# Kernel tuning notes

Hardware: AMD Instinct MI355X
Metric: run time of the kernel (lower is better)

## Reference

```python
import jax, jax.numpy as jnp
import numpy as np

K = 20  # neighbors, per get_u_xt default


def setup_inputs() -> dict:
    key = jax.random.key(0)
    ks = jax.random.split(key, 6)
    B, N, D, H = 2048, 100000, 64, 256
    return {
        "t": jax.random.uniform(ks[0], (1,), dtype=jnp.float32),
        "z": jax.random.normal(ks[1], (B, D + 2), dtype=jnp.float32),
        "data": jax.random.normal(ks[2], (N, D), dtype=jnp.float32),
        "velocity": jax.random.normal(ks[3], (N, D), dtype=jnp.float32),
        "W1": jax.random.normal(ks[4], (D + 1, H), dtype=jnp.float32) * 0.05,
        "b1": jnp.zeros((H,), dtype=jnp.float32),
        "W2": jax.random.normal(ks[5], (H, D), dtype=jnp.float32) * 0.05,
        "b2": jnp.zeros((D,), dtype=jnp.float32),
    }


def _get_u_xt(xt, x, v, k=K):
    # Euclidean cdist via ||a||^2 + ||b||^2 - 2 a.b  -> [B, N]
    sq = (jnp.sum(xt * xt, axis=1)[:, None]
          + jnp.sum(x * x, axis=1)[None, :]
          - 2.0 * (xt @ x.T))
    dists = jnp.sqrt(jnp.maximum(sq, 1e-30))
    neg_d, knn_idx = jax.lax.top_k(-dists, k)  # k smallest distances
    knn_dists = -neg_d                          # ascending order, [B, k]
    h = jnp.maximum(knn_dists[:, -1:], 1e-12)   # bandwidth = k-th NN dist
    w = jnp.exp(-knn_dists ** 2 / (2.0 * h ** 2))
    w = w / (jnp.sum(w, axis=1, keepdims=True) + 1e-12)
    v_knn = v[knn_idx]                          # gather [B, k, D]
    return jnp.einsum('bk,bkd->bd', w, v_knn)


def reference(t, z, data, velocity, W1, b1, W2, b2):
    x = z[:, :-2]                               # [B, D]
    B = x.shape[0]
    inp = jnp.concatenate([x, jnp.broadcast_to(t, (B,))[:, None]], axis=1)
    x_dot = jax.nn.relu(inp @ W1 + b1) @ W2 + b2  # MLP model(...) -> [B, D]
    u_t = _get_u_xt(x, data, velocity)
    eps = 1e-8  # torch F.cosine_similarity eps
    nu = jnp.maximum(jnp.linalg.norm(u_t, axis=1), eps)
    nx = jnp.maximum(jnp.linalg.norm(x_dot, axis=1), eps)
    cos_sim = 1.0 - jnp.sum(u_t * x_dot, axis=1) / (nu * nx)
    L2_squared = jnp.sum((u_t - x_dot) ** 2, axis=1)
    return jnp.concatenate([x_dot, cos_sim[:, None], L2_squared[:, None]], axis=1)
```

## Files before the change

kernel.cpp:

```cpp
#include <hip/hip_runtime.h>
#include <math.h>

#define B      2048
#define N      100000
#define NPAD2  100352
#define JGRP2  98
#define JT4    16
#define DD     64
#define HH     256
#define KK     20
#define SAMPLE 8192
#define CAP    1024
#define SSEL   512
#define SLACK  1.5f
#define LCAP   16

#define INF_F (__builtin_inff())

typedef __bf16 bf16x8 __attribute__((ext_vector_type(8)));
typedef __bf16 bf16x4 __attribute__((ext_vector_type(4)));
typedef float  floatx4 __attribute__((ext_vector_type(4)));
union U16 { uint4 u; bf16x8 v; };

__device__ __forceinline__ float wsum64(float v) {
    #pragma unroll
    for (int o = 32; o > 0; o >>= 1) v += __shfl_xor(v, o, 64);
    return v;
}
__device__ __forceinline__ int wsum64i(int v) {
    #pragma unroll
    for (int o = 32; o > 0; o >>= 1) v += __shfl_xor(v, o, 64);
    return v;
}

#define NB_DATA 6272
#define NB_PREP 512
#define NB_MLP  256
__global__ __launch_bounds__(256) void setup_all(const float* __restrict__ z,
                                                 const float* __restrict__ tp,
                                                 const float* __restrict__ data,
                                                 const float* __restrict__ W1,
                                                 const float* __restrict__ b1,
                                                 const float* __restrict__ W2,
                                                 const float* __restrict__ b2,
                                                 float* __restrict__ xs,
                                                 float* __restrict__ xnorm,
                                                 __bf16* __restrict__ xs_h,
                                                 int* __restrict__ cnt,
                                                 float* __restrict__ dnorm,
                                                 float* __restrict__ dnh,
                                                 __bf16* __restrict__ d_hi,
                                                 float* __restrict__ xdot) {
    int bx = blockIdx.x, tid = threadIdx.x;
    if (bx < NB_DATA) {
        int gt = bx * 256 + tid;
        int j = gt >> 4, l = gt & 15;
        float4 v = make_float4(0.f, 0.f, 0.f, 0.f);
        if (j < N)
            v = reinterpret_cast<const float4*>(data + (size_t)j * 64)[l];
        bf16x4 o;
        o.x = (__bf16)v.x; o.y = (__bf16)v.y; o.z = (__bf16)v.z; o.w = (__bf16)v.w;
        *reinterpret_cast<bf16x4*>(d_hi + (size_t)j * 64 + l * 4) = o;
        float s = v.x * v.x + v.y * v.y + v.z * v.z + v.w * v.w;
        #pragma unroll
        for (int o2 = 1; o2 < 16; o2 <<= 1) s += __shfl_xor(s, o2, 64);
        if (l == 0) {
            dnorm[j] = (j < N) ? s : INF_F;
            dnh[j]   = (j < N) ? 0.5f * s : INF_F;
        }
    } else if (bx < NB_DATA + NB_PREP) {
        int row = (bx - NB_DATA) * 4 + (tid >> 6);
        int d = tid & 63;
        float v = z[row * 66 + d];
        xs[row * 64 + d] = v;
        xs_h[row * 64 + d] = (__bf16)v;
        float s = wsum64(v * v);
        if (d == 0) xnorm[row] = s;
        if (d == 1) cnt[row] = 0;
    } else {
        __shared__ float sin_[8][65];
        __shared__ float shid[8][HH];
        int row0 = (bx - NB_DATA - NB_PREP) * 8;
        float tval = tp[0];
        for (int idx = tid; idx < 8 * 64; idx += 256) {
            int r = idx >> 6, d = idx & 63;
            sin_[r][d] = z[(row0 + r) * 66 + d];
        }
        if (tid < 8) sin_[tid][64] = tval;
        __syncthreads();
        int h = tid;
        float acc[8];
        #pragma unroll
        for (int r = 0; r < 8; ++r) acc[r] = b1[h];
        for (int i = 0; i < 65; ++i) {
            float wv = W1[i * HH + h];
            #pragma unroll
            for (int r = 0; r < 8; ++r) acc[r] = fmaf(sin_[r][i], wv, acc[r]);
        }
        #pragma unroll
        for (int r = 0; r < 8; ++r) shid[r][h] = fmaxf(acc[r], 0.f);
        __syncthreads();
        int d = tid & 63, rb = tid >> 6;
        for (int rr = rb; rr < 8; rr += 4) {
            float a = b2[d];
            #pragma unroll 8
            for (int hh2 = 0; hh2 < HH; ++hh2)
                a = fmaf(shid[rr][hh2], W2[hh2 * 64 + d], a);
            xdot[(size_t)(row0 + rr) * 64 + d] = a;
        }
    }
}

__global__ __launch_bounds__(256) void sample_gemm(const __bf16* __restrict__ xs_h,
                                                   const __bf16* __restrict__ d_hi,
                                                   const float* __restrict__ xnorm,
                                                   const float* __restrict__ dnorm,
                                                   unsigned short* __restrict__ samp16) {
    int tid = threadIdx.x;
    int m0 = blockIdx.x * 128;
    int jbase = blockIdx.y * 128;
    int wv = tid >> 6, wm = wv & 1, wn = wv >> 1;
    int lane = tid & 63, l16 = lane & 15, quad = lane >> 4;

    bf16x8 af[2][4], bfr[2][4];
    #pragma unroll
    for (int s = 0; s < 2; ++s)
        #pragma unroll
        for (int mt = 0; mt < 4; ++mt) {
            int row = m0 + wm * 64 + mt * 16 + l16;
            U16 u; u.u = reinterpret_cast<const uint4*>(xs_h + (size_t)row * 64)[s * 4 + quad];
            af[s][mt] = u.v;
        }
    #pragma unroll
    for (int s = 0; s < 2; ++s)
        #pragma unroll
        for (int nt = 0; nt < 4; ++nt) {
            int jr = jbase + wn * 64 + nt * 16 + l16;
            U16 u; u.u = reinterpret_cast<const uint4*>(d_hi + (size_t)jr * 64)[s * 4 + quad];
            bfr[s][nt] = u.v;
        }
    float dn[4], sxn[4][4];
    #pragma unroll
    for (int nt = 0; nt < 4; ++nt)
        dn[nt] = dnorm[jbase + wn * 64 + nt * 16 + l16];
    #pragma unroll
    for (int mt = 0; mt < 4; ++mt)
        #pragma unroll
        for (int rg = 0; rg < 4; ++rg)
            sxn[mt][rg] = xnorm[m0 + wm * 64 + mt * 16 + quad * 4 + rg];

    floatx4 acc[4][4];
    #pragma unroll
    for (int mt = 0; mt < 4; ++mt)
        #pragma unroll
        for (int nt = 0; nt < 4; ++nt)
            acc[mt][nt] = (floatx4){0.f, 0.f, 0.f, 0.f};
    #pragma unroll
    for (int s = 0; s < 2; ++s)
        #pragma unroll
        for (int mt = 0; mt < 4; ++mt)
            #pragma unroll
            for (int nt = 0; nt < 4; ++nt)
                acc[mt][nt] = __builtin_amdgcn_mfma_f32_16x16x32_bf16(
                    af[s][mt], bfr[s][nt], acc[mt][nt], 0, 0, 0);

    #pragma unroll
    for (int mt = 0; mt < 4; ++mt)
        #pragma unroll
        for (int nt = 0; nt < 4; ++nt) {
            floatx4 a4 = acc[mt][nt];
            int j = jbase + wn * 64 + nt * 16 + l16;
            #pragma unroll
            for (int rg = 0; rg < 4; ++rg) {
                int row = m0 + wm * 64 + mt * 16 + quad * 4 + rg;
                float sq = fmaf(a4[rg], -2.f, dn[nt]) + sxn[mt][rg];
                samp16[(size_t)row * SAMPLE + j] =
                    (unsigned short)(__float_as_uint(fmaxf(sq, 0.f)) >> 16);
            }
        }
}

__global__ __launch_bounds__(256) void thr_select(const unsigned short* __restrict__ samp16,
                                                  float* __restrict__ thr) {
    int wv = threadIdx.x >> 6, lane = threadIdx.x & 63;
    int row = blockIdx.x * 4 + wv;
    const unsigned* sp = reinterpret_cast<const unsigned*>(samp16 + (size_t)row * SAMPLE);
    unsigned w[64];
    #pragma unroll
    for (int i = 0; i < 64; ++i) w[i] = sp[lane + i * 64];
    unsigned res = 0;
    for (int b = 15; b >= 0; --b) {
        unsigned cand = res | (1u << b);
        int c = 0;
        #pragma unroll
        for (int i = 0; i < 64; ++i) {
            c += ((w[i] & 0xFFFFu) < cand);
            c += ((w[i] >> 16) < cand);
        }
        c = wsum64i(c);
        if (c <= KK - 1) res = cand;
    }
    if (lane == 0) thr[row] = __uint_as_float((res + 1u) << 16);
}

__global__ __launch_bounds__(256, 3) void gemm_filter(const __bf16* __restrict__ xs_h,
                                                      const __bf16* __restrict__ d_hi,
                                                      const float* __restrict__ xnorm,
                                                      const float* __restrict__ dnh,
                                                      const float* __restrict__ thr,
                                                      int* __restrict__ cnt,
                                                      float* __restrict__ bufd,
                                                      int* __restrict__ bufi) {
    __shared__ float sts[128];
    __shared__ int   lcnt[128];
    __shared__ float lbd[128][LCAP + 1];
    __shared__ int   lbj[128][LCAP + 1];
    int tid = threadIdx.x;
    int m0 = blockIdx.x * 128;
    int jstart = blockIdx.y * (JT4 * 64);
    int wv = tid >> 6, wm = wv & 1, wn = wv >> 1;
    int lane = tid & 63, l16 = lane & 15, quad = lane >> 4;

    if (tid < 128) {
        sts[tid] = thr[m0 + tid] + 2.0f * SLACK;
        lcnt[tid] = 0;
    }
    bf16x8 af[2][4];
    #pragma unroll
    for (int s = 0; s < 2; ++s)
        #pragma unroll
        for (int mt = 0; mt < 4; ++mt) {
            int row = m0 + wm * 64 + mt * 16 + l16;
            U16 u; u.u = reinterpret_cast<const uint4*>(xs_h + (size_t)row * 64)[s * 4 + quad];
            af[s][mt] = u.v;
        }
    float scv[4][4];
    #pragma unroll
    for (int mt = 0; mt < 4; ++mt)
        #pragma unroll
        for (int rg = 0; rg < 4; ++rg) {
            int mg = m0 + wm * 64 + mt * 16 + quad * 4 + rg;
            scv[mt][rg] = 0.5f * (thr[mg] + 2.0f * SLACK - xnorm[mg]);
        }
    __syncthreads();

    uint4 bb[2][4];
    float dh[2][2];
    {
        #pragma unroll
        for (int s = 0; s < 2; ++s)
            #pragma unroll
            for (int nt = 0; nt < 2; ++nt) {
                int jr = jstart + wn * 32 + nt * 16 + l16;
                bb[0][s * 2 + nt] = reinterpret_cast<const uint4*>(d_hi + (size_t)jr * 64)[s * 4 + quad];
            }
        #pragma unroll
        for (int nt = 0; nt < 2; ++nt)
            dh[0][nt] = dnh[jstart + wn * 32 + nt * 16 + l16];
    }

    #pragma unroll 2
    for (int t = 0; t < JT4; ++t) {
        int cur = t & 1, nxt = cur ^ 1;
        if (t + 1 < JT4) {
            int jb = jstart + (t + 1) * 64;
            #pragma unroll
            for (int s = 0; s < 2; ++s)
                #pragma unroll
                for (int nt = 0; nt < 2; ++nt) {
                    int jr = jb + wn * 32 + nt * 16 + l16;
                    bb[nxt][s * 2 + nt] = reinterpret_cast<const uint4*>(d_hi + (size_t)jr * 64)[s * 4 + quad];
                }
            #pragma unroll
            for (int nt = 0; nt < 2; ++nt)
                dh[nxt][nt] = dnh[jb + wn * 32 + nt * 16 + l16];
        }

        floatx4 acc[4][2];
        #pragma unroll
        for (int mt = 0; mt < 4; ++mt) {
            floatx4 cv = (floatx4){scv[mt][0], scv[mt][1], scv[mt][2], scv[mt][3]};
            acc[mt][0] = cv;
            acc[mt][1] = cv;
        }
        #pragma unroll
        for (int s = 0; s < 2; ++s) {
            U16 u0, u1;
            u0.u = bb[cur][s * 2 + 0];
            u1.u = bb[cur][s * 2 + 1];
            #pragma unroll
            for (int mt = 0; mt < 4; ++mt) {
                acc[mt][0] = __builtin_amdgcn_mfma_f32_16x16x32_bf16(af[s][mt], u0.v, acc[mt][0], 0, 0, 0);
                acc[mt][1] = __builtin_amdgcn_mfma_f32_16x16x32_bf16(af[s][mt], u1.v, acc[mt][1], 0, 0, 0);
            }
        }

        int jb = jstart + t * 64;
        #pragma unroll
        for (int nt = 0; nt < 2; ++nt) {
            int j = jb + wn * 32 + nt * 16 + l16;
            float dd = dh[cur][nt];
            #pragma unroll
            for (int mt = 0; mt < 4; ++mt) {
                floatx4 a4 = acc[mt][nt];
                bool p0 = a4[0] >= dd, p1 = a4[1] >= dd;
                bool p2 = a4[2] >= dd, p3 = a4[3] >= dd;
                if (p0 | p1 | p2 | p3) {
                    #pragma unroll
                    for (int rg = 0; rg < 4; ++rg) {
                        bool pp = (rg == 0) ? p0 : (rg == 1) ? p1 : (rg == 2) ? p2 : p3;
                        if (pp) {
                            int mloc = wm * 64 + mt * 16 + quad * 4 + rg;
                            float delta = 2.0f * (dd - a4[rg]);
                            int pos = atomicAdd(&lcnt[mloc], 1);
                            if (pos < LCAP) {
                                lbd[mloc][pos] = delta;
                                lbj[mloc][pos] = j;
                            } else {
                                int row = m0 + mloc;
                                int gp = atomicAdd(&cnt[row], 1);
                                if (gp < CAP) {
                                    bufd[(size_t)row * CAP + gp] = sts[mloc] + delta;
                                    bufi[(size_t)row * CAP + gp] = j;
                                }
                            }
                        }
                    }
                }
            }
        }
    }
    __syncthreads();
    if (tid < 128) {
        int c = lcnt[tid];
        if (c > LCAP) c = LCAP;
        if (c > 0) {
            int row = m0 + tid;
            float ts = sts[tid];
            int base = atomicAdd(&cnt[row], c);
            for (int i = 0; i < c; ++i) {
                int gp = base + i;
                if (gp < CAP) {
                    bufd[(size_t)row * CAP + gp] = ts + lbd[tid][i];
                    bufi[(size_t)row * CAP + gp] = lbj[tid][i];
                }
            }
        }
    }
}

__global__ __launch_bounds__(64) void select_finish(const float* __restrict__ bufd,
                                                    const int* __restrict__ bufi,
                                                    const int* __restrict__ cnt,
                                                    const float* __restrict__ xs,
                                                    const float* __restrict__ xnorm,
                                                    const float* __restrict__ dnorm,
                                                    const float* __restrict__ data,
                                                    const float* __restrict__ xdot,
                                                    const float* __restrict__ vel,
                                                    float* __restrict__ out) {
    __shared__ float sd[CAP];
    __shared__ int   si[CAP];
    __shared__ float sx[64];
    __shared__ float se[SSEL];
    __shared__ int   sj[SSEL];
    __shared__ int   scnt;
    __shared__ float seld[KK];
    __shared__ int   seli[KK];
    __shared__ float selw[KK];
    int row = blockIdx.x, lane = threadIdx.x;
    int n = cnt[row];
    if (n > CAP) n = CAP;
    for (int i = lane; i < n; i += 64) {
        sd[i] = bufd[(size_t)row * CAP + i];
        si[i] = bufi[(size_t)row * CAP + i];
    }
    sx[lane] = xs[row * 64 + lane];
    if (lane == 0) scnt = 0;
    __syncthreads();

    unsigned res = 0;
    for (int b = 30; b >= 0; --b) {
        unsigned cand = res | (1u << b);
        int c = 0;
        for (int i = lane; i < n; i += 64)
            c += (__float_as_uint(fmaxf(sd[i], 0.f)) < cand);
        c = wsum64i(c);
        if (c <= KK - 1) res = cand;
    }
    float T = __uint_as_float(res);

    for (int i = lane; i < n; i += 64) {
        if (sd[i] <= T + 2.0f * SLACK) {
            int q = atomicAdd(&scnt, 1);
            if (q < SSEL) sj[q] = si[i];
        }
    }
    __syncthreads();
    int m = scnt < SSEL ? scnt : SSEL;
    for (int c = lane; c < m; c += 64) {
        int j = sj[c];
        const float4* dp = reinterpret_cast<const float4*>(data + (size_t)j * 64);
        float dot = 0.f;
        #pragma unroll
        for (int kb = 0; kb < 16; ++kb) {
            float4 q = dp[kb];
            dot = fmaf(sx[kb * 4 + 0], q.x, dot);
            dot = fmaf(sx[kb * 4 + 1], q.y, dot);
            dot = fmaf(sx[kb * 4 + 2], q.z, dot);
            dot = fmaf(sx[kb * 4 + 3], q.w, dot);
        }
        se[c] = xnorm[row] + dnorm[j] - 2.0f * dot;
    }
    __syncthreads();
    for (int k = 0; k < KK; ++k) {
        float v = INF_F; int id = 0x7fffffff; int p = -1;
        for (int i = lane; i < m; i += 64) {
            float x = se[i]; int xi = sj[i];
            if (x < v || (x == v && xi < id)) { v = x; id = xi; p = i; }
        }
        #pragma unroll
        for (int o = 32; o > 0; o >>= 1) {
            float ov = __shfl_xor(v, o, 64);
            int oid = __shfl_xor(id, o, 64);
            int op  = __shfl_xor(p, o, 64);
            if (ov < v || (ov == v && oid < id)) { v = ov; id = oid; p = op; }
        }
        if (lane == 0) {
            seld[k] = v; seli[k] = id;
            if (p >= 0) se[p] = INF_F;
        }
        __syncthreads();
    }
    float d20 = sqrtf(fmaxf(seld[KK - 1], 1e-30f));
    float h = fmaxf(d20, 1e-12f);
    float wk = 0.f;
    if (lane < KK) {
        float dd = sqrtf(fmaxf(seld[lane], 1e-30f));
        wk = expf(-(dd * dd) / (2.f * h * h));
    }
    float tot = wsum64(wk) + 1e-12f;
    if (lane < KK) selw[lane] = wk / tot;
    __syncthreads();
    float u = 0.f;
    #pragma unroll
    for (int k = 0; k < KK; ++k)
        u = fmaf(selw[k], vel[(size_t)seli[k] * 64 + lane], u);
    float xd = xdot[(size_t)row * 64 + lane];
    float du  = wsum64(u * xd);
    float nu2 = wsum64(u * u);
    float nx2 = wsum64(xd * xd);
    float l2  = wsum64((u - xd) * (u - xd));
    float nu = fmaxf(sqrtf(nu2), 1e-8f);
    float nx = fmaxf(sqrtf(nx2), 1e-8f);
    out[(size_t)row * 66 + lane] = xd;
    if (lane == 0) {
        out[(size_t)row * 66 + 64] = 1.f - du / (nu * nx);
        out[(size_t)row * 66 + 65] = l2;
    }
}

extern "C" void kernel_launch(void* const* d_in, const int* in_sizes, int n_in,
                              void* d_out, int out_size, void* d_ws, size_t ws_size,
                              hipStream_t stream) {
    const float* t_   = (const float*)d_in[0];
    const float* z    = (const float*)d_in[1];
    const float* data = (const float*)d_in[2];
    const float* vel  = (const float*)d_in[3];
    const float* W1   = (const float*)d_in[4];
    const float* b1   = (const float*)d_in[5];
    const float* W2   = (const float*)d_in[6];
    const float* b2   = (const float*)d_in[7];
    float* out = (float*)d_out;

    float*  xs    = (float*)d_ws;
    float*  xnorm = xs + 131072;
    float*  thr   = xnorm + 2048;
    int*    cnt   = (int*)(thr + 2048);
    float*  xdot  = (float*)(cnt + 2048);
    float*  dnorm = xdot + 131072;
    float*  dnh   = dnorm + NPAD2;
    __bf16* xs_h  = (__bf16*)(dnh + NPAD2);
    __bf16* d_hi  = xs_h + 131072;
    unsigned short* samp16 = (unsigned short*)(d_hi + (size_t)NPAD2 * 64);
    float*  bufd  = (float*)samp16;
    int*    bufi  = (int*)(bufd + (size_t)B * CAP);

    setup_all<<<NB_DATA + NB_PREP + NB_MLP, 256, 0, stream>>>(
        z, t_, data, W1, b1, W2, b2, xs, xnorm, xs_h, cnt, dnorm, dnh, d_hi, xdot);
    sample_gemm<<<dim3(B / 128, SAMPLE / 128), 256, 0, stream>>>(xs_h, d_hi, xnorm, dnorm, samp16);
    thr_select<<<B / 4, 256, 0, stream>>>(samp16, thr);
    gemm_filter<<<dim3(B / 128, JGRP2), 256, 0, stream>>>(
        xs_h, d_hi, xnorm, dnh, thr, cnt, bufd, bufi);
    select_finish<<<B, 64, 0, stream>>>(bufd, bufi, cnt, xs, xnorm, dnorm, data,
                                        xdot, vel, out);
    (void)ws_size; (void)in_sizes; (void)n_in; (void)out_size;
}
```

Baseline: 300.4 us.

## Stage data tiles through LDS ring buffer with async global-to-LDS loads

Replaces the register double-buffered B-tile loads in the filter GEMM with a 3-deep LDS ring filled by global_load_lds, using a swizzled layout and explicit vmcnt waits and barriers. The dnh norms are also staged into LDS. LCAP is halved to shrink LDS use and occupancy is raised to 4 blocks per SM, and MFMA sections get raised scheduling priority. This aims to hide global load latency behind the MFMA and filter work, at the cost of extra barriers per tile and more spills to the global buffer when the local buffer is smaller. An unused helper function filter_step holding dead placeholder code is also added.

```diff
diff --git a/kernel.cpp b/kernel.cpp
--- a/kernel.cpp
+++ b/kernel.cpp
@@ -13,7 +13,8 @@
 #define CAP    1024
 #define SSEL   512
 #define SLACK  1.5f
-#define LCAP   16
+#define LCAP   8
+#define RING_D 3
 
 #define INF_F (__builtin_inff())
 
@@ -31,6 +32,12 @@
     #pragma unroll
     for (int o = 32; o > 0; o >>= 1) v += __shfl_xor(v, o, 64);
     return v;
+}
+
+__device__ __forceinline__ void glds16(const void* g, void* l) {
+    __builtin_amdgcn_global_load_lds(
+        (const __attribute__((address_space(1))) unsigned*)g,
+        (__attribute__((address_space(3))) unsigned*)l, 16, 0, 0);
 }
 
 #define NB_DATA 6272
@@ -203,7 +210,68 @@
     if (lane == 0) thr[row] = __uint_as_float((res + 1u) << 16);
 }
 
-__global__ __launch_bounds__(256, 3) void gemm_filter(const __bf16* __restrict__ xs_h,
+__device__ __forceinline__ void filter_step(
+    const char* ringslot, const float* sdnh, int t, int jstart, int m0,
+    int wn, int l16, int jr0, const int off16[2][2],
+    const bf16x8 af[2][4], const float scv[4][4],
+    const float* sts, int* lcnt, float (*lbd)[LCAP + 1], int (*lbj)[LCAP + 1],
+    int* __restrict__ cnt, float* __restrict__ bufd, int* __restrict__ bufi) {
+    const uint4* bsrc = reinterpret_cast<const uint4*>(ringslot);
+    U16 u00, u01, u10, u11;
+    u00.u = bsrc[off16[0][0]];
+    u01.u = bsrc[off16[0][1]];
+    u10.u = bsrc[off16[1][0]];
+    u11.u = bsrc[off16[1][1]];
+    float dd0 = sdnh[t * 64 + jr0];
+    float dd1 = sdnh[t * 64 + jr0 + 16];
+
+    floatx4 acc[4][2];
+    #pragma unroll
+    for (int mt = 0; mt < 4; ++mt) {
+        floatx4 cv = (floatx4){scv[mt][0], scv[mt][1], scv[mt][2], scv[mt][3]};
+        acc[mt][0] = cv;
+        acc[mt][1] = cv;
+    }
+    __builtin_amdgcn_s_setprio(1);
+    #pragma unroll
+    for (int mt = 0; mt < 4; ++mt) {
+        acc[mt][0] = __builtin_amdgcn_mfma_f32_16x16x32_bf16(af[0][mt], u00.v, acc[mt][0], 0, 0, 0);
+        acc[mt][1] = __builtin_amdgcn_mfma_f32_16x16x32_bf16(af[0][mt], u01.v, acc[mt][1], 0, 0, 0);
+    }
+    #pragma unroll
+    for (int mt = 0; mt < 4; ++mt) {
+        acc[mt][0] = __builtin_amdgcn_mfma_f32_16x16x32_bf16(af[1][mt], u10.v, acc[mt][0], 0, 0, 0);
+        acc[mt][1] = __builtin_amdgcn_mfma_f32_16x16x32_bf16(af[1][mt], u11.v, acc[mt][1], 0, 0, 0);
+    }
+    __builtin_amdgcn_s_setprio(0);
+
+    int jb = jstart + t * 64;
+    int wm_mloc = 0;
+    (void)wm_mloc;
+    #pragma unroll
+    for (int nt = 0; nt < 2; ++nt) {
+        int j = jb + wn * 32 + nt * 16 + l16;
+        float dd = nt ? dd1 : dd0;
+        #pragma unroll
+        for (int mt = 0; mt < 4; ++mt) {
+            floatx4 a4 = acc[mt][nt];
+            float mx = fmaxf(fmaxf(a4[0], a4[1]), fmaxf(a4[2], a4[3]));
+            if (mx >= dd) {
+                #pragma unroll
+                for (int rg = 0; rg < 4; ++rg) {
+                    if (a4[rg] >= dd) {
+                        int mloc = ((off16[0][0] >> 31) & 0);
+                        (void)mloc;
+                        int mrow = (int)(sts - sts); (void)mrow;
+                    }
+                }
+            }
+        }
+    }
+}
+
+
+__global__ __launch_bounds__(256, 4) void gemm_filter(const __bf16* __restrict__ xs_h,
                                                       const __bf16* __restrict__ d_hi,
                                                       const float* __restrict__ xnorm,
                                                       const float* __restrict__ dnh,
@@ -215,6 +283,9 @@
     __shared__ int   lcnt[128];
     __shared__ float lbd[128][LCAP + 1];
     __shared__ int   lbj[128][LCAP + 1];
+    __shared__ __align__(16) char  ring[RING_D * 8192];
+    __shared__ __align__(16) float sdnh[JT4 * 64];
+
     int tid = threadIdx.x;
     int m0 = blockIdx.x * 128;
     int jstart = blockIdx.y * (JT4 * 64);
@@ -242,86 +313,104 @@
             int mg = m0 + wm * 64 + mt * 16 + quad * 4 + rg;
             scv[mt][rg] = 0.5f * (thr[mg] + 2.0f * SLACK - xnorm[mg]);
         }
-    __syncthreads();
-
-    uint4 bb[2][4];
-    float dh[2][2];
-    {
-        #pragma unroll
-        for (int s = 0; s < 2; ++s)
+
+    int r8 = lane >> 3, c8 = lane & 7;
+    const char* gB = (const char*)d_hi + (size_t)jstart * 128
+                   + (size_t)(wv * 2048 + r8 * 128 + ((c8 ^ r8) << 4));
+    int off16[2][2];
+    #pragma unroll
+    for (int s = 0; s < 2; ++s)
+        #pragma unroll
+        for (int nt = 0; nt < 2; ++nt) {
+            int row = wn * 32 + nt * 16 + l16;
+            off16[s][nt] = row * 8 + ((s * 4 + quad) ^ (l16 & 7));
+        }
+    int jr0 = wn * 32 + l16;
+
+    asm volatile("" ::: "memory");
+
+    glds16((const char*)dnh + (size_t)jstart * 4 + (size_t)(wv * 1024 + lane * 16),
+           (char*)sdnh + wv * 1024);
+    #pragma unroll
+    for (int p = 0; p < 2; ++p) {
+        glds16(gB + (size_t)p * 8192,        ring + p * 8192 + wv * 2048);
+        glds16(gB + (size_t)p * 8192 + 1024, ring + p * 8192 + wv * 2048 + 1024);
+    }
+    asm volatile("s_waitcnt lgkmcnt(0)" ::: "memory");
+
+    int sc = 0;
+    int sp = 2;
+    for (int t = 0; t < JT4; ++t) {
+        if (t < JT4 - 2) {
+            __builtin_amdgcn_s_barrier();
+            asm volatile("" ::: "memory");
+            glds16(gB + (size_t)(t + 2) * 8192,        ring + sp * 8192 + wv * 2048);
+            glds16(gB + (size_t)(t + 2) * 8192 + 1024, ring + sp * 8192 + wv * 2048 + 1024);
+            asm volatile("s_waitcnt vmcnt(4)" ::: "memory");
+        } else if (t == JT4 - 2) {
+            asm volatile("s_waitcnt vmcnt(2)" ::: "memory");
+        } else {
+            asm volatile("s_waitcnt vmcnt(0)" ::: "memory");
+        }
+        __builtin_amdgcn_s_barrier();
+        asm volatile("" ::: "memory");
+
+        {
+            const uint4* bsrc = reinterpret_cast<const uint4*>(ring + sc * 8192);
+            U16 u00, u01, u10, u11;
+            u00.u = bsrc[off16[0][0]];
+            u01.u = bsrc[off16[0][1]];
+            u10.u = bsrc[off16[1][0]];
+            u11.u = bsrc[off16[1][1]];
+            float dd0 = sdnh[t * 64 + jr0];
+            float dd1 = sdnh[t * 64 + jr0 + 16];
+
+            floatx4 acc[4][2];
+            #pragma unroll
+            for (int mt = 0; mt < 4; ++mt) {
+                floatx4 cv = (floatx4){scv[mt][0], scv[mt][1], scv[mt][2], scv[mt][3]};
+                acc[mt][0] = cv;
+                acc[mt][1] = cv;
+            }
+            __builtin_amdgcn_s_setprio(1);
+            #pragma unroll
+            for (int mt = 0; mt < 4; ++mt) {
+                acc[mt][0] = __builtin_amdgcn_mfma_f32_16x16x32_bf16(af[0][mt], u00.v, acc[mt][0], 0, 0, 0);
+                acc[mt][1] = __builtin_amdgcn_mfma_f32_16x16x32_bf16(af[0][mt], u01.v, acc[mt][1], 0, 0, 0);
+            }
+            #pragma unroll
+            for (int mt = 0; mt < 4; ++mt) {
+                acc[mt][0] = __builtin_amdgcn_mfma_f32_16x16x32_bf16(af[1][mt], u10.v, acc[mt][0], 0, 0, 0);
+                acc[mt][1] = __builtin_amdgcn_mfma_f32_16x16x32_bf16(af[1][mt], u11.v, acc[mt][1], 0, 0, 0);
+            }
+            __builtin_amdgcn_s_setprio(0);
+
+            int jb = jstart + t * 64;
             #pragma unroll
             for (int nt = 0; nt < 2; ++nt) {
-                int jr = jstart + wn * 32 + nt * 16 + l16;
-                bb[0][s * 2 + nt] = reinterpret_cast<const uint4*>(d_hi + (size_t)jr * 64)[s * 4 + quad];
-            }
-        #pragma unroll
-        for (int nt = 0; nt < 2; ++nt)
-            dh[0][nt] = dnh[jstart + wn * 32 + nt * 16 + l16];
-    }
-
-    #pragma unroll 2
-    for (int t = 0; t < JT4; ++t) {
-        int cur = t & 1, nxt = cur ^ 1;
-        if (t + 1 < JT4) {
-            int jb = jstart + (t + 1) * 64;
-            #pragma unroll
-            for (int s = 0; s < 2; ++s)
+                int j = jb + wn * 32 + nt * 16 + l16;
+                float dd = nt ? dd1 : dd0;
                 #pragma unroll
-                for (int nt = 0; nt < 2; ++nt) {
-                    int jr = jb + wn * 32 + nt * 16 + l16;
-                    bb[nxt][s * 2 + nt] = reinterpret_cast<const uint4*>(d_hi + (size_t)jr * 64)[s * 4 + quad];
-                }
-            #pragma unroll
-            for (int nt = 0; nt < 2; ++nt)
-                dh[nxt][nt] = dnh[jb + wn * 32 + nt * 16 + l16];
-        }
-
-        floatx4 acc[4][2];
-        #pragma unroll
-        for (int mt = 0; mt < 4; ++mt) {
-            floatx4 cv = (floatx4){scv[mt][0], scv[mt][1], scv[mt][2], scv[mt][3]};
-            acc[mt][0] = cv;
-            acc[mt][1] = cv;
-        }
-        #pragma unroll
-        for (int s = 0; s < 2; ++s) {
-            U16 u0, u1;
-            u0.u = bb[cur][s * 2 + 0];
-            u1.u = bb[cur][s * 2 + 1];
-            #pragma unroll
-            for (int mt = 0; mt < 4; ++mt) {
-                acc[mt][0] = __builtin_amdgcn_mfma_f32_16x16x32_bf16(af[s][mt], u0.v, acc[mt][0], 0, 0, 0);
-                acc[mt][1] = __builtin_amdgcn_mfma_f32_16x16x32_bf16(af[s][mt], u1.v, acc[mt][1], 0, 0, 0);
-            }
-        }
-
-        int jb = jstart + t * 64;
-        #pragma unroll
-        for (int nt = 0; nt < 2; ++nt) {
-            int j = jb + wn * 32 + nt * 16 + l16;
-            float dd = dh[cur][nt];
-            #pragma unroll
-            for (int mt = 0; mt < 4; ++mt) {
-                floatx4 a4 = acc[mt][nt];
-                bool p0 = a4[0] >= dd, p1 = a4[1] >= dd;
-                bool p2 = a4[2] >= dd, p3 = a4[3] >= dd;
-                if (p0 | p1 | p2 | p3) {
-                    #pragma unroll
-                    for (int rg = 0; rg < 4; ++rg) {
-                        bool pp = (rg == 0) ? p0 : (rg == 1) ? p1 : (rg == 2) ? p2 : p3;
-                        if (pp) {
-                            int mloc = wm * 64 + mt * 16 + quad * 4 + rg;
-                            float delta = 2.0f * (dd - a4[rg]);
-                            int pos = atomicAdd(&lcnt[mloc], 1);
-                            if (pos < LCAP) {
-                                lbd[mloc][pos] = delta;
-                                lbj[mloc][pos] = j;
-                            } else {
-                                int row = m0 + mloc;
-                                int gp = atomicAdd(&cnt[row], 1);
-                                if (gp < CAP) {
-                                    bufd[(size_t)row * CAP + gp] = sts[mloc] + delta;
-                                    bufi[(size_t)row * CAP + gp] = j;
+                for (int mt = 0; mt < 4; ++mt) {
+                    floatx4 a4 = acc[mt][nt];
+                    float mx = fmaxf(fmaxf(a4[0], a4[1]), fmaxf(a4[2], a4[3]));
+                    if (mx >= dd) {
+                        #pragma unroll
+                        for (int rg = 0; rg < 4; ++rg) {
+                            if (a4[rg] >= dd) {
+                                int mloc = wm * 64 + mt * 16 + quad * 4 + rg;
+                                float delta = 2.0f * (dd - a4[rg]);
+                                int pos = atomicAdd(&lcnt[mloc], 1);
+                                if (pos < LCAP) {
+                                    lbd[mloc][pos] = delta;
+                                    lbj[mloc][pos] = j;
+                                } else {
+                                    int row = m0 + mloc;
+                                    int gp = atomicAdd(&cnt[row], 1);
+                                    if (gp < CAP) {
+                                        bufd[(size_t)row * CAP + gp] = sts[mloc] + delta;
+                                        bufi[(size_t)row * CAP + gp] = j;
+                                    }
                                 }
                             }
                         }
@@ -329,6 +418,8 @@
                 }
             }
         }
+        sp = (sp == RING_D - 1) ? 0 : sp + 1;
+        sc = (sc == RING_D - 1) ? 0 : sc + 1;
     }
     __syncthreads();
     if (tid < 128) {
```

Result: slower. 309.1 us (+2.9%).
